# Kernel tuning notes

Hardware: AMD Instinct MI355X
Metric: run time of the kernel (lower is better)

Reference implementation:

```python
import jax, jax.numpy as jnp
import numpy as np

B, S, D = 4, 2048, 1024  # batch, seq_len, model dim (= qk_dim = output_dim)


def setup_inputs() -> dict:
    key = jax.random.key(0)
    kq, kk, kv, kwq, kwk, kwv = jax.random.split(key, 6)
    q = jax.random.normal(kq, (B, S, D), dtype=jnp.float32)
    k = jax.random.normal(kk, (B, S, D), dtype=jnp.float32)
    v = jax.random.normal(kv, (B, S, D), dtype=jnp.float32)
    # causal mask, broadcast over batch
    mask = jnp.broadcast_to(jnp.tril(jnp.ones((S, S), dtype=bool)), (B, S, S))
    W_q = jax.random.uniform(kwq, (D, D), dtype=jnp.float32)
    W_k = jax.random.uniform(kwk, (D, D), dtype=jnp.float32)
    W_v = jax.random.uniform(kwv, (D, D), dtype=jnp.float32)
    return {"q": q, "k": k, "v": v, "mask": mask, "W_q": W_q, "W_k": W_k, "W_v": W_v}


def reference(q, k, v, mask, W_q, W_k, W_v):
    q1 = q @ W_q  # (B, S, D)
    k1 = k @ W_k  # (B, S, D)
    v1 = v @ W_v  # (B, S, D)
    qk = jnp.einsum('bij,bkj->bik', q1, k1)  # (B, S, S)
    qk = qk * jax.lax.rsqrt(float(k1.shape[-1]))
    neg_inf = jnp.finfo(jnp.float32).min
    qk = jnp.where(mask, qk, neg_inf)
    s = jax.nn.softmax(qk, axis=-1)
    return jnp.einsum('bij,bjk->bik', s, v1)
```

## Files before the change

### kernel.cpp

```cpp
#include <hip/hip_runtime.h>
#include <hip/hip_bf16.h>
#include <float.h>


typedef __attribute__((ext_vector_type(8))) short bf16x8;
typedef __attribute__((ext_vector_type(4))) float f32x4;

#define MFMA16 __builtin_amdgcn_mfma_f32_16x16x32_bf16

union U8 { bf16x8 v; unsigned w[4]; };

__device__ __forceinline__ ushort f2bf(float x) {
  union { float f; unsigned u; } v; v.f = x;
  unsigned r = v.u + 0x7fffu + ((v.u >> 16) & 1u);
  return (ushort)(r >> 16);
}
__device__ __forceinline__ float bf2f(ushort h) {
  union { unsigned u; float f; } v; v.u = ((unsigned)h) << 16;
  return v.f;
}
__device__ __forceinline__ void splitf(float x, ushort& hi, ushort& lo) {
  hi = f2bf(x);
  lo = f2bf(x - bf2f(hi));
}

__device__ __forceinline__ bf16x8 cvt8(const float* lp) {
  U8 H;
#pragma unroll
  for (int p = 0; p < 4; ++p) {
    const unsigned u0 = __float_as_uint(lp[2 * p]);
    const unsigned u1 = __float_as_uint(lp[2 * p + 1]);
    const unsigned r0 = (u0 + 0x7fffu + ((u0 >> 16) & 1u)) >> 16;
    const unsigned r1 = (u1 + 0x7fffu + ((u1 >> 16) & 1u)) & 0xffff0000u;
    H.w[p] = r0 | r1;
  }
  return H.v;
}

#define GLOAD16(gp, lp)                                                        \
  __builtin_amdgcn_global_load_lds(                                            \
      (const __attribute__((address_space(1))) void*)(gp),                     \
      (__attribute__((address_space(3))) void*)(lp), 16, 0, 0)

#define BARRIER() asm volatile("s_barrier" ::: "memory")
#define VMCNT4() asm volatile("s_waitcnt vmcnt(4)" ::: "memory")

__device__ __forceinline__ void stage_bf16_32(const ushort* g, int pitch,
                                              ushort* lds, int w, int lane) {
#pragma unroll
  for (int i = 0; i < 2; ++i) {
    const int c = w * 2 + i;
    const int row = c * 16 + (lane >> 2);
    const int kp = (lane & 3) * 8;
    GLOAD16(g + (size_t)row * pitch + kp, lds + c * 512);
  }
}
__device__ __forceinline__ void stage_bf16_64(const ushort* g, int pitch,
                                              ushort* lds, int w, int lane) {
#pragma unroll
  for (int i = 0; i < 4; ++i) {
    const int c = w * 4 + i;
    const int row = c * 8 + (lane >> 3);
    const int kp = (lane & 7) * 8;
    GLOAD16(g + (size_t)row * pitch + kp, lds + c * 512);
  }
}
__device__ __forceinline__ void stage_bf16_64x64(const ushort* g, int pitch,
                                                 ushort* lds, int w, int lane) {
#pragma unroll
  for (int i = 0; i < 2; ++i) {
    const int c = w * 2 + i;
    const int row = c * 8 + (lane >> 3);
    const int kp = (lane & 7) * 8;
    GLOAD16(g + (size_t)row * pitch + kp, lds + c * 512);
  }
}
__device__ __forceinline__ void stage_f32_32(const float* g, int pitch,
                                             float* lds, int w, int lane) {
#pragma unroll
  for (int i = 0; i < 4; ++i) {
    const int c = w * 4 + i;
    const int row = c * 8 + (lane >> 3);
    const int kp = (lane & 7) * 4;
    GLOAD16(g + (size_t)row * pitch + kp, lds + c * 256);
  }
}

__device__ __forceinline__ void stage_half8(const ushort* __restrict__ g,
                                            ushort* lds, int k0, int t) {
#pragma unroll
  for (int i = 0; i < 2; ++i) {
    const int c = t + i * 512;
    const int row = c >> 3;
    const int pcb = (c & 7) * 16;
    const int lcb = pcb ^ (((row >> 2) & 3) << 5);
    GLOAD16(g + (size_t)row * 1024 + k0 + (lcb >> 1), lds + c * 8);
  }
}

__global__ __launch_bounds__(256) void wt_split(
    const float* __restrict__ q, const float* __restrict__ k,
    const float* __restrict__ W0, const float* __restrict__ W1,
    const float* __restrict__ W2, ushort* __restrict__ Th0,
    ushort* __restrict__ Tl0, ushort* __restrict__ Th1,
    ushort* __restrict__ Tl1, ushort* __restrict__ Th2,
    ushort* __restrict__ qh, ushort* __restrict__ ql,
    ushort* __restrict__ kh, ushort* __restrict__ kl) {
  __shared__ float t[32][33];
  const int f = blockIdx.x;
  if (f < 3072) {
    const int z = f >> 10, r10 = f & 1023;
    const int bx = r10 & 31, by = r10 >> 5;
    const float* W = z == 0 ? W0 : (z == 1 ? W1 : W2);
    ushort* Th = z == 0 ? Th0 : (z == 1 ? Th1 : Th2);
    ushort* Tl = z == 0 ? Tl0 : (z == 1 ? Tl1 : nullptr);
    const int r = threadIdx.x >> 3, c4 = (threadIdx.x & 7) * 4;
    const float4 x = *reinterpret_cast<const float4*>(
        &W[(size_t)(bx * 32 + r) * 1024 + by * 32 + c4]);
    t[r][c4] = x.x; t[r][c4 + 1] = x.y; t[r][c4 + 2] = x.z; t[r][c4 + 3] = x.w;
    __syncthreads();
    ushort h[4], l[4];
#pragma unroll
    for (int j = 0; j < 4; ++j) splitf(t[c4 + j][r], h[j], l[j]);
    const size_t o = (size_t)(by * 32 + r) * 1024 + bx * 32 + c4;
    *reinterpret_cast<ushort4*>(&Th[o]) = ushort4{h[0], h[1], h[2], h[3]};
    if (Tl)
      *reinterpret_cast<ushort4*>(&Tl[o]) = ushort4{l[0], l[1], l[2], l[3]};
  } else {
    const int fl = f - 3072;
    const float* X = (fl >> 11) ? k : q;
    ushort* H = (fl >> 11) ? kh : qh;
    ushort* L = (fl >> 11) ? kl : ql;
    const int n4 = 2097152;
    for (int i = (fl & 2047) * 256 + threadIdx.x; i < n4; i += 2048 * 256) {
      const float4 x = reinterpret_cast<const float4*>(X)[i];
      ushort h0, l0, h1, l1, h2, l2, h3, l3;
      splitf(x.x, h0, l0); splitf(x.y, h1, l1);
      splitf(x.z, h2, l2); splitf(x.w, h3, l3);
      reinterpret_cast<ushort4*>(H)[i] = ushort4{h0, h1, h2, h3};
      reinterpret_cast<ushort4*>(L)[i] = ushort4{l0, l1, l2, l3};
    }
  }
}

__global__ __launch_bounds__(512, 2) void proj_qk8(
    const ushort* __restrict__ Ah0, const ushort* __restrict__ Al0,
    const ushort* __restrict__ Ah1, const ushort* __restrict__ Al1,
    const ushort* __restrict__ Bh0, const ushort* __restrict__ Bl0,
    const ushort* __restrict__ Bh1, const ushort* __restrict__ Bl1,
    ushort* __restrict__ Oh0, ushort* __restrict__ Ol0,
    ushort* __restrict__ Oh1, ushort* __restrict__ Ol1) {
  __shared__ ushort As[2][16384];
  __shared__ ushort Bs[2][16384];
  const int bid = blockIdx.x;
  const int fid = (bid & 7) * 32 + (bid >> 3);
  const int z = fid >> 7, r = fid & 127;
  const int yt = r >> 2, xt = r & 3;
  const ushort* Ah = z ? Ah1 : Ah0;
  const ushort* Al = z ? Al1 : Al0;
  const ushort* Bh = z ? Bh1 : Bh0;
  const ushort* Bl = z ? Bl1 : Bl0;
  ushort* Oh = z ? Oh1 : Oh0;
  ushort* Ol = z ? Ol1 : Ol0;
  const size_t am0 = (size_t)yt * 256 * 1024;
  const size_t bn0 = (size_t)xt * 256 * 1024;
  const int t = threadIdx.x;
  const int lane = t & 63, w = t >> 6;
  const int wm = w >> 2, wn = w & 3;
  const int lr = lane & 15, kg = lane >> 4;
  f32x4 acc[8][4] = {};
  bf16x8 Ar[4][2], Br[4][2];

  auto stage_unit = [&](int kt, int u) {
    if (kt >= 48) kt -= 48;
    const int seg = kt >> 4;
    const int k0 = (kt & 15) * 64;
    const int slot = kt & 1;
    const int h = u & 1;
    if (u < 2) {
      const ushort* g = ((seg == 1) ? Al : Ah) + am0 + (size_t)(h * 128) * 1024;
      stage_half8(g, &As[slot][h * 8192], k0, t);
    } else {
      const ushort* g = ((seg == 2) ? Bl : Bh) + bn0 + (size_t)(h * 128) * 1024;
      stage_half8(g, &Bs[slot][h * 8192], k0, t);
    }
  };
  auto loadA = [&](int slot, int mq) {
#pragma unroll
    for (int m = 0; m < 4; ++m)
#pragma unroll
      for (int ks = 0; ks < 2; ++ks) {
        const int row = wm * 128 + (mq * 4 + m) * 16 + lr;
        const int cb = (ks * 64 + kg * 16) ^ (((row >> 2) & 3) << 5);
        Ar[m][ks] =
            *reinterpret_cast<const bf16x8*>(&As[slot][row * 64 + (cb >> 1)]);
      }
  };
  auto loadB = [&](int slot, int nq) {
#pragma unroll
    for (int n = 0; n < 2; ++n)
#pragma unroll
      for (int ks = 0; ks < 2; ++ks) {
        const int col = wn * 64 + (nq * 2 + n) * 16 + lr;
        const int cb = (ks * 64 + kg * 16) ^ (((col >> 2) & 3) << 5);
        Br[nq * 2 + n][ks] =
            *reinterpret_cast<const bf16x8*>(&Bs[slot][col * 64 + (cb >> 1)]);
      }
  };
  auto mfma_q = [&](int mq, int nq) {
    __builtin_amdgcn_s_setprio(1);
#pragma unroll
    for (int m = 0; m < 4; ++m)
#pragma unroll
      for (int n = 0; n < 2; ++n)
#pragma unroll
        for (int ks = 0; ks < 2; ++ks)
          acc[mq * 4 + m][nq * 2 + n] = MFMA16(
              Ar[m][ks], Br[nq * 2 + n][ks], acc[mq * 4 + m][nq * 2 + n], 0, 0, 0);
    __builtin_amdgcn_s_setprio(0);
  };

  stage_unit(0, 0); stage_unit(0, 1); stage_unit(0, 2); stage_unit(0, 3);
  stage_unit(1, 0);

  for (int it = 0; it < 24; ++it) {
    const int kt1 = 2 * it + 1;
    stage_unit(kt1, 1);
    VMCNT4(); BARRIER();
    loadA(0, 0); loadB(0, 0);
    mfma_q(0, 0);
    BARRIER();
    stage_unit(kt1, 2);
    BARRIER();
    loadB(0, 1);
    mfma_q(0, 1);
    BARRIER();
    stage_unit(kt1, 3);
    BARRIER();
    loadA(0, 1);
    mfma_q(1, 0);
    BARRIER();
    stage_unit(kt1 + 1, 0);
    BARRIER();
    mfma_q(1, 1);
    BARRIER();
    stage_unit(kt1 + 1, 1);
    VMCNT4(); BARRIER();
    loadA(1, 0); loadB(1, 0);
    mfma_q(0, 0);
    BARRIER();
    stage_unit(kt1 + 1, 2);
    BARRIER();
    loadB(1, 1);
    mfma_q(0, 1);
    BARRIER();
    stage_unit(kt1 + 1, 3);
    BARRIER();
    loadA(1, 1);
    mfma_q(1, 0);
    BARRIER();
    stage_unit(kt1 + 2, 0);
    BARRIER();
    mfma_q(1, 1);
    BARRIER();
  }

#pragma unroll
  for (int m = 0; m < 8; ++m)
#pragma unroll
    for (int n = 0; n < 4; ++n)
#pragma unroll
      for (int reg = 0; reg < 4; ++reg) {
        const int gm = yt * 256 + wm * 128 + m * 16 + kg * 4 + reg;
        const int gn = xt * 256 + wn * 64 + n * 16 + lr;
        ushort h, l;
        splitf(acc[m][n][reg], h, l);
        Oh[(size_t)gm * 1024 + gn] = h;
        Ol[(size_t)gm * 1024 + gn] = l;
      }
}

__global__ __launch_bounds__(256) void qk2(
    const ushort* __restrict__ q1h, const ushort* __restrict__ q1l,
    const ushort* __restrict__ k1h, const ushort* __restrict__ k1l,
    float* __restrict__ scoresA, float* __restrict__ scoresB) {
  __shared__ ushort Ahs[4096], Als[4096], Bhs[4096], Bls[4096];
  const int f = blockIdx.x;
  const int s = (f & 7) * 136 + (f >> 3);
  const int z = s / 544;
  const int rem = s % 544;
  const int b = rem / 136;
  int p = rem % 136, ti = 0, accp = 0;
  while (accp + ti + 1 <= p) { accp += ti + 1; ++ti; }
  const int tj = p - accp;
  const int tid = threadIdx.x, lane = tid & 63, w = tid >> 6;
  const int wr = w >> 1, wc = w & 1;
  const int lr = lane & 15, kg = lane >> 4;
  const int kh0 = z * 512;
  const ushort* qh = q1h + ((size_t)b * 2048 + ti * 128) * 1024 + kh0;
  const ushort* ql = q1l + ((size_t)b * 2048 + ti * 128) * 1024 + kh0;
  const ushort* kh = k1h + ((size_t)b * 2048 + tj * 128) * 1024 + kh0;
  const ushort* kl = k1l + ((size_t)b * 2048 + tj * 128) * 1024 + kh0;
  f32x4 acc[4][4] = {};

  for (int k0 = 0; k0 < 512; k0 += 32) {
    stage_bf16_32(qh + k0, 1024, Ahs, w, lane);
    stage_bf16_32(ql + k0, 1024, Als, w, lane);
    stage_bf16_32(kh + k0, 1024, Bhs, w, lane);
    stage_bf16_32(kl + k0, 1024, Bls, w, lane);
    __syncthreads();
    bf16x8 ah[4], al[4], bh[4], bl[4];
#pragma unroll
    for (int m = 0; m < 4; ++m) {
      ah[m] = *reinterpret_cast<bf16x8*>(&Ahs[(wr * 64 + m * 16 + lr) * 32 + kg * 8]);
      al[m] = *reinterpret_cast<bf16x8*>(&Als[(wr * 64 + m * 16 + lr) * 32 + kg * 8]);
    }
#pragma unroll
    for (int n = 0; n < 4; ++n) {
      bh[n] = *reinterpret_cast<bf16x8*>(&Bhs[(wc * 64 + n * 16 + lr) * 32 + kg * 8]);
      bl[n] = *reinterpret_cast<bf16x8*>(&Bls[(wc * 64 + n * 16 + lr) * 32 + kg * 8]);
    }
#pragma unroll
    for (int m = 0; m < 4; ++m)
#pragma unroll
      for (int n = 0; n < 4; ++n) {
        acc[m][n] = MFMA16(ah[m], bh[n], acc[m][n], 0, 0, 0);
        acc[m][n] = MFMA16(ah[m], bl[n], acc[m][n], 0, 0, 0);
        acc[m][n] = MFMA16(al[m], bh[n], acc[m][n], 0, 0, 0);
      }
    __syncthreads();
  }
  const float sc = 0.03125f;
  float* st = (z ? scoresB : scoresA) + ((size_t)b * 136 + p) * 16384;
#pragma unroll
  for (int m = 0; m < 4; ++m)
#pragma unroll
    for (int n = 0; n < 4; ++n)
#pragma unroll
      for (int reg = 0; reg < 4; ++reg) {
        const int il = wr * 64 + m * 16 + kg * 4 + reg;
        const int jl = wc * 64 + n * 16 + lr;
        st[il * 128 + jl] = acc[m][n][reg] * sc;
      }
}

__global__ __launch_bounds__(256) void sm_projv(
    float* __restrict__ scoresA, const float* __restrict__ scoresB,
    const ushort* __restrict__ Wvt, const float* __restrict__ V,
    ushort* __restrict__ v1t) {
  __shared__ __align__(16) char smem[24576];
  const int tid = threadIdx.x, lane = tid & 63, w = tid >> 6;
  const int fg = blockIdx.x;
  if (fg < 8192) {
    float* red = reinterpret_cast<float*>(smem);
    const int b = fg >> 11, r = fg & 2047;
    const int ti = r >> 7, rl = r & 127, ncol = (ti + 1) * 128;
    const int valid = r + 1;
    const size_t tbase = ((size_t)b * 136 + (ti * (ti + 1)) / 2) * 16384;
    float* srowA = scoresA + tbase;
    const float* srowB = scoresB + tbase;

    float vals[2][4];
    float mx = -FLT_MAX;
#pragma unroll
    for (int c = 0; c < 2; ++c) {
      const int j = tid * 4 + c * 1024;
      const size_t o = (size_t)(j >> 7) * 16384 + rl * 128 + (j & 127);
      const float4 a = *reinterpret_cast<const float4*>(srowA + o);
      const float4 bb = *reinterpret_cast<const float4*>(srowB + o);
      vals[c][0] = (j + 0 < valid) ? a.x + bb.x : -FLT_MAX;
      vals[c][1] = (j + 1 < valid) ? a.y + bb.y : -FLT_MAX;
      vals[c][2] = (j + 2 < valid) ? a.z + bb.z : -FLT_MAX;
      vals[c][3] = (j + 3 < valid) ? a.w + bb.w : -FLT_MAX;
      mx = fmaxf(mx, fmaxf(fmaxf(vals[c][0], vals[c][1]),
                           fmaxf(vals[c][2], vals[c][3])));
    }
#pragma unroll
    for (int o = 32; o; o >>= 1) mx = fmaxf(mx, __shfl_xor(mx, o));
    if (lane == 0) red[w] = mx;
    __syncthreads();
    mx = fmaxf(fmaxf(red[0], red[1]), fmaxf(red[2], red[3]));

    float ex[2][4];
    float sum = 0.f;
#pragma unroll
    for (int c = 0; c < 2; ++c)
#pragma unroll
      for (int e = 0; e < 4; ++e) {
        const int j = tid * 4 + c * 1024 + e;
        ex[c][e] = (j < valid) ? __expf(vals[c][e] - mx) : 0.f;
        sum += ex[c][e];
      }
#pragma unroll
    for (int o = 32; o; o >>= 1) sum += __shfl_xor(sum, o);
    if (lane == 0) red[4 + w] = sum;
    __syncthreads();
    sum = red[4] + red[5] + red[6] + red[7];
    const float inv = 1.f / sum;
#pragma unroll
    for (int c = 0; c < 2; ++c) {
      const int j = tid * 4 + c * 1024;
      if (j < ncol) {
        ushort* pt =
            reinterpret_cast<ushort*>(srowA + (size_t)(j >> 7) * 16384);
        ushort4 pw;
        pw.x = f2bf(ex[c][0] * inv); pw.y = f2bf(ex[c][1] * inv);
        pw.z = f2bf(ex[c][2] * inv); pw.w = f2bf(ex[c][3] * inv);
        *reinterpret_cast<ushort4*>(&pt[rl * 256 + (j & 127)]) = pw;
      }
    }
  } else {
    ushort* Ahs = reinterpret_cast<ushort*>(smem);
    float* Bs = reinterpret_cast<float*>(smem + 8192);
    const int f2 = fg - 8192;
    const int yb = (f2 >> 3) & 7;
    const int xb = (f2 & 7) + ((f2 >> 6) << 3);
    const int wr = w >> 1, wc = w & 1;
    const int lr = lane & 15, kg = lane >> 4;
    const int m0 = yb * 128;
    const int n0 = xb * 128;
    f32x4 acc[4][4] = {};

    for (int k0 = 0; k0 < 1024; k0 += 32) {
      stage_bf16_32(Wvt + (size_t)m0 * 1024 + k0, 1024, Ahs, w, lane);
      stage_f32_32(V + (size_t)n0 * 1024 + k0, 1024, Bs, w, lane);
      __syncthreads();
      bf16x8 ah[4], bh[4];
#pragma unroll
      for (int m = 0; m < 4; ++m)
        ah[m] = *reinterpret_cast<bf16x8*>(
            &Ahs[(wr * 64 + m * 16 + lr) * 32 + kg * 8]);
#pragma unroll
      for (int n = 0; n < 4; ++n)
        bh[n] = cvt8(&Bs[(wc * 64 + n * 16 + lr) * 32 + kg * 8]);
#pragma unroll
      for (int m = 0; m < 4; ++m)
#pragma unroll
        for (int n = 0; n < 4; ++n)
          acc[m][n] = MFMA16(ah[m], bh[n], acc[m][n], 0, 0, 0);
      __syncthreads();
    }
#pragma unroll
    for (int m = 0; m < 4; ++m)
#pragma unroll
      for (int n = 0; n < 4; ++n)
#pragma unroll
        for (int reg = 0; reg < 4; ++reg) {
          const int gm = m0 + wr * 64 + m * 16 + kg * 4 + reg;
          const int gn = n0 + wc * 64 + n * 16 + lr;
          const int b = gn >> 11, jj = gn & 2047;
          v1t[((size_t)b << 21) + (size_t)gm * 2048 + jj] = f2bf(acc[m][n][reg]);
        }
  }
}

__global__ __launch_bounds__(256) void pv2(const float* __restrict__ scores,
                                           const ushort* __restrict__ v1t,
                                           float* __restrict__ out) {
  __shared__ ushort Ps[128 * 64], Vs[64 * 64];
  const int fl = blockIdx.x;
  const int s = (fl & 7) * 128 + (fl >> 3);
  const int b = s >> 8, rem = s & 255;
  const int ti = 15 - (rem >> 4);
  const int n0 = (rem & 15) * 64;
  const int tid = threadIdx.x, lane = tid & 63, w = tid >> 6;
  const int wr = w >> 1, wc = w & 1;
  const int lr = lane & 15, kg = lane >> 4;
  const int tri_ti = (ti * (ti + 1)) / 2;
  const ushort* vbase = v1t + ((size_t)b << 21) + (size_t)n0 * 2048;
  const int kend = (ti + 1) * 128;
  f32x4 acc[4][2] = {};

  for (int k0 = 0; k0 < kend; k0 += 64) {
    const ushort* pt = reinterpret_cast<const ushort*>(
        scores + ((size_t)b * 136 + tri_ti + (k0 >> 7)) * 16384);
    stage_bf16_64(pt + (k0 & 64), 256, Ps, w, lane);
    stage_bf16_64x64(vbase + k0, 2048, Vs, w, lane);
    __syncthreads();
#pragma unroll
    for (int t2 = 0; t2 < 2; ++t2) {
      bf16x8 pa[4], vb[2];
#pragma unroll
      for (int m = 0; m < 4; ++m)
        pa[m] = *reinterpret_cast<bf16x8*>(
            &Ps[(wr * 64 + m * 16 + lr) * 64 + t2 * 32 + kg * 8]);
#pragma unroll
      for (int n = 0; n < 2; ++n)
        vb[n] = *reinterpret_cast<bf16x8*>(
            &Vs[(wc * 32 + n * 16 + lr) * 64 + t2 * 32 + kg * 8]);
#pragma unroll
      for (int m = 0; m < 4; ++m)
#pragma unroll
        for (int n = 0; n < 2; ++n)
          acc[m][n] = MFMA16(pa[m], vb[n], acc[m][n], 0, 0, 0);
    }
    __syncthreads();
  }
#pragma unroll
  for (int m = 0; m < 4; ++m)
#pragma unroll
    for (int n = 0; n < 2; ++n)
#pragma unroll
      for (int reg = 0; reg < 4; ++reg) {
        const int gm = ti * 128 + wr * 64 + m * 16 + kg * 4 + reg;
        const int gn = n0 + wc * 32 + n * 16 + lr;
        out[((size_t)b * 2048 + gm) * 1024 + gn] = acc[m][n][reg];
      }
}

extern "C" void kernel_launch(void* const* d_in, const int* in_sizes, int n_in,
                              void* d_out, int out_size, void* d_ws,
                              size_t ws_size, hipStream_t stream) {
  const float* q = (const float*)d_in[0];
  const float* k = (const float*)d_in[1];
  const float* v = (const float*)d_in[2];
  const float* Wq = (const float*)d_in[4];
  const float* Wk = (const float*)d_in[5];
  const float* Wv = (const float*)d_in[6];
  float* out = (float*)d_out;

  char* ws = (char*)d_ws;
  const size_t SCORES_T = 35651584;
  float* scoresA = (float*)ws;
  float* scoresB = (float*)(ws + SCORES_T);
  ushort* qsh = (ushort*)ws;
  ushort* qsl = qsh + 8388608;
  ushort* ksh = qsh + 2 * 8388608;
  ushort* ksl = qsh + 3 * 8388608;
  ushort* q1hi = (ushort*)(ws + 2 * SCORES_T);
  ushort* q1lo = q1hi + 8388608;
  ushort* k1hi = q1hi + 2 * 8388608;
  ushort* k1lo = q1hi + 3 * 8388608;
  ushort* v1t = (ushort*)(ws + 2 * SCORES_T);
  ushort* Wqth = (ushort*)(ws + 2 * SCORES_T + 67108864);
  ushort* Wqtl = Wqth + 1048576;
  ushort* Wkth = Wqth + 2097152;
  ushort* Wktl = Wqth + 3145728;
  ushort* Wvt  = Wqth + 4194304;
  const size_t need = 2 * SCORES_T + 67108864 + 10485760;
  if (ws_size < need) return;

  dim3 blk(256);
  wt_split<<<dim3(7168), blk, 0, stream>>>(q, k, Wq, Wk, Wv, Wqth, Wqtl, Wkth,
                                           Wktl, Wvt, qsh, qsl, ksh, ksl);
  proj_qk8<<<dim3(256), dim3(512), 0, stream>>>(qsh, qsl, ksh, ksl, Wqth,
                                                Wqtl, Wkth, Wktl, q1hi, q1lo,
                                                k1hi, k1lo);
  qk2<<<dim3(1088), blk, 0, stream>>>(q1hi, q1lo, k1hi, k1lo, scoresA,
                                      scoresB);
  sm_projv<<<dim3(8704), blk, 0, stream>>>(scoresA, scoresB, Wvt, v, v1t);
  pv2<<<dim3(1024), blk, 0, stream>>>(scoresA, v1t, out);
}
```

Baseline: 316.6 us.

## Restructure projection GEMM into whole-tile double buffering with one barrier per step

Replaces the fine-grained schedule, which staged a quarter tile between MFMA quarters with eight barriers per k-tile, with a simple double-buffered loop. Each step issues the full A/B load for the next k-tile, waits with vmcnt(8), runs all four MFMA quarters and then hits a single barrier. It also changes the LDS XOR swizzle to (row&7)<<4 in both the staging and fragment-read paths to cut bank conflicts. Global load traffic now comes in larger bursts and overlaps less evenly with compute, and the last iteration issues a redundant wrap-around load.

```diff
diff --git a/kernel.cpp b/kernel.cpp
--- a/kernel.cpp
+++ b/kernel.cpp
@@ -43,7 +43,7 @@
       (__attribute__((address_space(3))) void*)(lp), 16, 0, 0)
 
 #define BARRIER() asm volatile("s_barrier" ::: "memory")
-#define VMCNT4() asm volatile("s_waitcnt vmcnt(4)" ::: "memory")
+#define VMCNT8() asm volatile("s_waitcnt vmcnt(8)" ::: "memory")
 
 __device__ __forceinline__ void stage_bf16_32(const ushort* g, int pitch,
                                               ushort* lds, int w, int lane) {
@@ -93,7 +93,7 @@
     const int c = t + i * 512;
     const int row = c >> 3;
     const int pcb = (c & 7) * 16;
-    const int lcb = pcb ^ (((row >> 2) & 3) << 5);
+    const int lcb = pcb ^ ((row & 7) << 4);
     GLOAD16(g + (size_t)row * 1024 + k0 + (lcb >> 1), lds + c * 8);
   }
 }
@@ -171,19 +171,19 @@
   f32x4 acc[8][4] = {};
   bf16x8 Ar[4][2], Br[4][2];
 
-  auto stage_unit = [&](int kt, int u) {
+  auto stage_tile = [&](int kt) {
     if (kt >= 48) kt -= 48;
     const int seg = kt >> 4;
     const int k0 = (kt & 15) * 64;
     const int slot = kt & 1;
-    const int h = u & 1;
-    if (u < 2) {
-      const ushort* g = ((seg == 1) ? Al : Ah) + am0 + (size_t)(h * 128) * 1024;
-      stage_half8(g, &As[slot][h * 8192], k0, t);
-    } else {
-      const ushort* g = ((seg == 2) ? Bl : Bh) + bn0 + (size_t)(h * 128) * 1024;
-      stage_half8(g, &Bs[slot][h * 8192], k0, t);
-    }
+    const ushort* ga = (seg == 1) ? Al : Ah;
+    const ushort* gb = (seg == 2) ? Bl : Bh;
+#pragma unroll
+    for (int h = 0; h < 2; ++h)
+      stage_half8(ga + am0 + (size_t)(h * 128) * 1024, &As[slot][h * 8192], k0, t);
+#pragma unroll
+    for (int h = 0; h < 2; ++h)
+      stage_half8(gb + bn0 + (size_t)(h * 128) * 1024, &Bs[slot][h * 8192], k0, t);
   };
   auto loadA = [&](int slot, int mq) {
 #pragma unroll
@@ -191,7 +191,7 @@
 #pragma unroll
       for (int ks = 0; ks < 2; ++ks) {
         const int row = wm * 128 + (mq * 4 + m) * 16 + lr;
-        const int cb = (ks * 64 + kg * 16) ^ (((row >> 2) & 3) << 5);
+        const int cb = (ks * 64 + kg * 16) ^ ((row & 7) << 4);
         Ar[m][ks] =
             *reinterpret_cast<const bf16x8*>(&As[slot][row * 64 + (cb >> 1)]);
       }
@@ -202,7 +202,7 @@
 #pragma unroll
       for (int ks = 0; ks < 2; ++ks) {
         const int col = wn * 64 + (nq * 2 + n) * 16 + lr;
-        const int cb = (ks * 64 + kg * 16) ^ (((col >> 2) & 3) << 5);
+        const int cb = (ks * 64 + kg * 16) ^ ((col & 7) << 4);
         Br[nq * 2 + n][ks] =
             *reinterpret_cast<const bf16x8*>(&Bs[slot][col * 64 + (cb >> 1)]);
       }
@@ -220,47 +220,19 @@
     __builtin_amdgcn_s_setprio(0);
   };
 
-  stage_unit(0, 0); stage_unit(0, 1); stage_unit(0, 2); stage_unit(0, 3);
-  stage_unit(1, 0);
-
-  for (int it = 0; it < 24; ++it) {
-    const int kt1 = 2 * it + 1;
-    stage_unit(kt1, 1);
-    VMCNT4(); BARRIER();
-    loadA(0, 0); loadB(0, 0);
+  stage_tile(0);
+#pragma unroll 2
+  for (int kt = 0; kt < 48; ++kt) {
+    const int slot = kt & 1;
+    stage_tile(kt + 1);
+    VMCNT8();
+    BARRIER();
+    loadA(slot, 0); loadB(slot, 0);
     mfma_q(0, 0);
-    BARRIER();
-    stage_unit(kt1, 2);
-    BARRIER();
-    loadB(0, 1);
+    loadB(slot, 1);
     mfma_q(0, 1);
-    BARRIER();
-    stage_unit(kt1, 3);
-    BARRIER();
-    loadA(0, 1);
+    loadA(slot, 1);
     mfma_q(1, 0);
-    BARRIER();
-    stage_unit(kt1 + 1, 0);
-    BARRIER();
-    mfma_q(1, 1);
-    BARRIER();
-    stage_unit(kt1 + 1, 1);
-    VMCNT4(); BARRIER();
-    loadA(1, 0); loadB(1, 0);
-    mfma_q(0, 0);
-    BARRIER();
-    stage_unit(kt1 + 1, 2);
-    BARRIER();
-    loadB(1, 1);
-    mfma_q(0, 1);
-    BARRIER();
-    stage_unit(kt1 + 1, 3);
-    BARRIER();
-    loadA(1, 1);
-    mfma_q(1, 0);
-    BARRIER();
-    stage_unit(kt1 + 2, 0);
-    BARRIER();
     mfma_q(1, 1);
     BARRIER();
   }
```

Measured after the change: 308.7 us. -2.5%, faster.
